# Kernel optimization log

Measured on AMD Instinct MI355X. Metric: run time of the kernel, lower is better.

The kernel has to match this reference:

```python
import jax, jax.numpy as jnp
import numpy as np

TOPK = 16  # matches selected per (frame, query pixel)


def setup_inputs() -> dict:
    key = jax.random.key(0)
    ks = jax.random.split(key, 4)
    B, T, N, C = 2, 3, 4096, 256  # batch, ref frames, 64x64 tokens, channels
    scale = 1.0 / np.sqrt(C)
    return {
        "tgt": jax.random.normal(ks[0], (B, N, C), dtype=jnp.float32),
        "ref": jax.random.normal(ks[1], (B, T, N, C), dtype=jnp.float32),
        "Wq": jax.random.normal(ks[2], (C, C), dtype=jnp.float32) * scale,
        "bq": jnp.zeros((C,), dtype=jnp.float32),
        "Wk": jax.random.normal(ks[3], (C, C), dtype=jnp.float32) * scale,
        "bk": jnp.zeros((C,), dtype=jnp.float32),
    }


def _l2norm(x, eps=1e-12):
    return x * jax.lax.rsqrt(jnp.sum(x * x, axis=-1, keepdims=True) + eps)


def reference(tgt, ref, Wq, bq, Wk, bk):
    # tgt: [B, Nq, C] target-frame tokens; ref: [B, T, Nr, C] reference-frame tokens
    B, Nq, C = tgt.shape
    T, Nr = ref.shape[1], ref.shape[2]
    q = _l2norm(tgt @ Wq + bq)                      # [B, Nq, C]
    k = _l2norm(ref @ Wk + bk)                      # [B, T, Nr, C]
    # cross-frame cosine-similarity correlation volume
    sim = jnp.einsum("bqc,btrc->btqr", q, k)        # [B, T, Nq, Nr]
    # top-k matched reference locations per query pixel
    topv, topi = jax.lax.top_k(sim, TOPK)           # [B, T, Nq, K]
    # gather matched reference features (irregular gather)
    bi = jnp.arange(B)[:, None, None, None]
    ti = jnp.arange(T)[None, :, None, None]
    gathered = ref[bi, ti, topi]                    # [B, T, Nq, K, C]
    # attention-weighted aggregation of matched features
    w = jax.nn.softmax(topv, axis=-1)               # [B, T, Nq, K]
    out = jnp.einsum("btqk,btqkc->btqc", w, gathered)  # [B, T, Nq, C]
    return out
```

## Files before the change

### kernel.cpp

```cpp
#include <hip/hip_runtime.h>
#include <stdint.h>

#define T_FRAMES 3
#define NTOK 4096
#define CH 256

typedef __attribute__((ext_vector_type(8))) short bf16x8;
typedef __attribute__((ext_vector_type(4))) float f32x4;
typedef __attribute__((address_space(1))) void gvoid;
typedef __attribute__((address_space(3))) void svoid;

__device__ __forceinline__ unsigned short f2bf_rne(float f) {
  union { float f; uint32_t u; } c; c.f = f;
  uint32_t u = c.u;
  return (unsigned short)((u + 0x7FFFu + ((u >> 16) & 1u)) >> 16);
}
__device__ __forceinline__ float bflo(uint32_t x) { return __uint_as_float(x << 16); }
__device__ __forceinline__ float bfhi(uint32_t x) { return __uint_as_float(x & 0xFFFF0000u); }

__global__ __launch_bounds__(256) void proj_kernel(
    const float* __restrict__ Xq, const float* __restrict__ Wq, const float* __restrict__ bq,
    const float* __restrict__ Xk, const float* __restrict__ Wk, const float* __restrict__ bk,
    unsigned short* __restrict__ Qb, float* __restrict__ Qlo,
    unsigned short* __restrict__ Kb, float* __restrict__ Klo)
{
  __shared__ double At[64][32];
  const int tid = threadIdx.x;
  int blk = blockIdx.x;
  const float *X, *W, *bias; unsigned short* Pb; float* Plo;
  if (blk < 256) { X = Xq; W = Wq; bias = bq; Pb = Qb; Plo = Qlo; }
  else           { X = Xk; W = Wk; bias = bk; Pb = Kb; Plo = Klo; blk -= 256; }
  const int rbase = blk * 32;
  const int wv = tid >> 6, lane = tid & 63;
  const int r0 = wv * 8;
  const int c4 = lane * 4;

  double acc[8][4];
  #pragma unroll
  for (int i = 0; i < 8; i++) {
    #pragma unroll
    for (int j = 0; j < 4; j++) acc[i][j] = (double)bias[c4 + j];
  }

  const int srow = tid & 31, skq = (tid >> 5) * 8;
  for (int kc = 0; kc < CH; kc += 64) {
    {
      const float* xp = X + (size_t)(rbase + srow) * CH + kc + skq;
      const float4 v0 = *(const float4*)(xp);
      const float4 v1 = *(const float4*)(xp + 4);
      At[skq + 0][srow] = (double)v0.x; At[skq + 1][srow] = (double)v0.y;
      At[skq + 2][srow] = (double)v0.z; At[skq + 3][srow] = (double)v0.w;
      At[skq + 4][srow] = (double)v1.x; At[skq + 5][srow] = (double)v1.y;
      At[skq + 6][srow] = (double)v1.z; At[skq + 7][srow] = (double)v1.w;
    }
    __syncthreads();
    #pragma unroll 8
    for (int k = 0; k < 64; k++) {
      const float4 w4 = *(const float4*)(W + (size_t)(kc + k) * CH + c4);
      const double b0 = (double)w4.x, b1 = (double)w4.y;
      const double b2 = (double)w4.z, b3 = (double)w4.w;
      double a[8];
      #pragma unroll
      for (int i = 0; i < 4; i++) {
        const double2 ap = *(const double2*)&At[k][r0 + 2 * i];
        a[2*i] = ap.x; a[2*i+1] = ap.y;
      }
      #pragma unroll
      for (int i = 0; i < 8; i++) {
        acc[i][0] += a[i] * b0; acc[i][1] += a[i] * b1;
        acc[i][2] += a[i] * b2; acc[i][3] += a[i] * b3;
      }
    }
    __syncthreads();
  }

  #pragma unroll
  for (int i = 0; i < 8; i++) {
    double ss = acc[i][0]*acc[i][0] + acc[i][1]*acc[i][1]
              + acc[i][2]*acc[i][2] + acc[i][3]*acc[i][3];
    #pragma unroll
    for (int off = 32; off >= 1; off >>= 1) ss += __shfl_xor(ss, off);
    const double inv = 1.0 / sqrt(ss + 1e-12);
    const size_t base = (size_t)(rbase + r0 + i) * CH + c4;
    double vd[4]; float fb[4]; unsigned short us[4];
    #pragma unroll
    for (int j = 0; j < 4; j++) {
      vd[j] = acc[i][j] * inv;
      us[j] = f2bf_rne((float)vd[j]);
      fb[j] = __uint_as_float(((uint32_t)us[j]) << 16);
    }
    uint2 pk; pk.x = (uint32_t)us[0] | ((uint32_t)us[1] << 16);
    pk.y = (uint32_t)us[2] | ((uint32_t)us[3] << 16);
    *(uint2*)(Pb + base) = pk;
    float4 lo;
    lo.x = (float)(vd[0] - (double)fb[0]); lo.y = (float)(vd[1] - (double)fb[1]);
    lo.z = (float)(vd[2] - (double)fb[2]); lo.w = (float)(vd[3] - (double)fb[3]);
    *(float4*)(Plo + base) = lo;
  }
}

__global__ __launch_bounds__(256, 4) void sim_cand_kernel(
    const unsigned short* __restrict__ Qb,
    const unsigned short* __restrict__ Kb,
    uint32_t* __restrict__ cand)
{
  __shared__ unsigned short kst[2][32 * 256];
  const int bid = blockIdx.x;
  const int rs = bid & 3;
  const int qb = (bid >> 2) & 63;
  const int bt = bid >> 8;
  const int b = bt / T_FRAMES;
  const int tid = threadIdx.x;
  const int wv = tid >> 6, lane = tid & 63;
  const int lq = lane & 15, g = lane >> 4;
  const int q = qb * 64 + wv * 16 + lq;

  bf16x8 bfr[8];
  {
    const unsigned short* qrow = Qb + (size_t)(b * NTOK + q) * CH + g * 8;
    #pragma unroll
    for (int kc = 0; kc < 8; kc++) bfr[kc] = *(const bf16x8*)(qrow + kc * 32);
  }
  uint32_t best[16];
  #pragma unroll
  for (int i = 0; i < 16; i++) best[i] = 0u;
  uint32_t s[16];

  const unsigned short* kbase = Kb + ((size_t)bt * NTOK + (size_t)rs * 1024) * CH;

#define STAGE(C, BUFI)                                                          \
  {                                                                             \
    _Pragma("unroll")                                                           \
    for (int t = 0; t < 4; t++) {                                               \
      const int o16 = (wv * 4 + t) * 64 + lane;                                 \
      const int row = o16 >> 5, colp = o16 & 31;                                \
      const int col16 = (colp - row) & 31;                                      \
      const unsigned short* gsrc = kbase + (size_t)((C) * 32 + row) * CH + col16 * 8; \
      __builtin_amdgcn_global_load_lds((const gvoid*)gsrc,                      \
          (svoid*)(&kst[BUFI][0] + (size_t)(wv * 4 + t) * 512), 16, 0, 0);      \
    }                                                                           \
  }

#define COMPUTE_HALF(CBASE, BUFI, SOFF)                                         \
  {                                                                             \
    _Pragma("unroll")                                                           \
    for (int t = 0; t < 2; t++) {                                               \
      f32x4 acc = {2.0f, 2.0f, 2.0f, 2.0f};                                     \
      const int arow = t * 16 + lq;                                             \
      const unsigned short* rowp = &kst[BUFI][0] + (size_t)arow * 256;          \
      _Pragma("unroll")                                                         \
      for (int kc = 0; kc < 8; kc++) {                                          \
        const int colp = (kc * 4 + g + arow) & 31;                              \
        const bf16x8 a = *(const bf16x8*)(rowp + colp * 8);                     \
        acc = __builtin_amdgcn_mfma_f32_16x16x32_bf16(a, bfr[kc], acc, 0, 0, 0);\
      }                                                                         \
      _Pragma("unroll")                                                         \
      for (int j = 0; j < 4; j++) {                                             \
        const uint32_t bits = __float_as_uint(acc[j]);                          \
        s[(SOFF) + t * 4 + j] = (bits & 0xFFFFFC00u) |                          \
            (uint32_t)((CBASE) * 32 + t * 16 + g * 4 + j);                      \
      }                                                                         \
    }                                                                           \
  }

#define SORT16_MERGE()                                                          \
  {                                                                             \
    _Pragma("unroll")                                                           \
    for (int bk = 2; bk <= 16; bk <<= 1) {                                      \
      _Pragma("unroll")                                                         \
      for (int bj = bk >> 1; bj > 0; bj >>= 1) {                                \
        _Pragma("unroll")                                                       \
        for (int i = 0; i < 16; i++) {                                          \
          const int l = i ^ bj;                                                 \
          if (l > i) {                                                          \
            const bool up = ((i & bk) != 0);                                    \
            const uint32_t a2 = s[i], b2 = s[l];                                \
            const uint32_t mn = a2 < b2 ? a2 : b2;                              \
            const uint32_t mx = a2 < b2 ? b2 : a2;                              \
            s[i] = up ? mn : mx; s[l] = up ? mx : mn;                           \
          }                                                                     \
        }                                                                       \
      }                                                                         \
    }                                                                           \
    uint32_t m[16];                                                             \
    _Pragma("unroll")                                                           \
    for (int i = 0; i < 16; i++) {                                              \
      const uint32_t a2 = best[i], b2 = s[15 - i];                              \
      m[i] = a2 > b2 ? a2 : b2;                                                 \
    }                                                                           \
    _Pragma("unroll")                                                           \
    for (int bj = 8; bj > 0; bj >>= 1) {                                        \
      _Pragma("unroll")                                                         \
      for (int i = 0; i < 16; i++) {                                            \
        const int l = i ^ bj;                                                   \
        if (l > i) {                                                            \
          const uint32_t a2 = m[i], b2 = m[l];                                  \
          const uint32_t mn = a2 < b2 ? a2 : b2;                                \
          const uint32_t mx = a2 < b2 ? b2 : a2;                                \
          m[i] = mx; m[l] = mn;                                                 \
        }                                                                       \
      }                                                                         \
    }                                                                           \
    _Pragma("unroll")                                                           \
    for (int i = 0; i < 16; i++) best[i] = m[i];                                \
  }

  STAGE(0, 0);
  __syncthreads();
  for (int cp = 0; cp < 16; cp++) {
    const int c0 = 2 * cp;
    STAGE(c0 + 1, 1);
    COMPUTE_HALF(c0, 0, 0);
    __syncthreads();
    if (cp < 15) STAGE(c0 + 2, 0);
    COMPUTE_HALF(c0 + 1, 1, 8);
    SORT16_MERGE();
    __syncthreads();
  }

  #pragma unroll
  for (int st = 16; st <= 32; st <<= 1) {
    uint32_t o[16];
    #pragma unroll
    for (int i = 0; i < 16; i++) o[i] = (uint32_t)__shfl_xor((int)best[15 - i], st);
    #pragma unroll
    for (int i = 0; i < 16; i++) best[i] = best[i] > o[i] ? best[i] : o[i];
    #pragma unroll
    for (int bj = 8; bj > 0; bj >>= 1) {
      #pragma unroll
      for (int i = 0; i < 16; i++) {
        const int l = i ^ bj;
        if (l > i) {
          const uint32_t a2 = best[i], b2 = best[l];
          const uint32_t mn = a2 < b2 ? a2 : b2;
          const uint32_t mx = a2 < b2 ? b2 : a2;
          best[i] = mx; best[l] = mn;
        }
      }
    }
  }
  if (g == 0) {
    uint32_t* cp2 = cand + ((size_t)bt * NTOK + q) * 64 + rs * 16;
    #pragma unroll
    for (int i = 0; i < 16; i += 4) {
      uint4 v; v.x = best[i]; v.y = best[i+1]; v.z = best[i+2]; v.w = best[i+3];
      *(uint4*)(cp2 + i) = v;
    }
  }
#undef STAGE
#undef COMPUTE_HALF
#undef SORT16_MERGE
}

__global__ __launch_bounds__(256) void out_kernel(
    const unsigned short* __restrict__ Qb, const float* __restrict__ Qlo,
    const unsigned short* __restrict__ Kb, const float* __restrict__ Klo,
    const uint32_t* __restrict__ cand, const float* __restrict__ ref,
    float* __restrict__ out)
{
  const int tid = threadIdx.x, wv = tid >> 6, lane = tid & 63;
  const int rowid = blockIdx.x * 4 + wv;
  const int bt = rowid >> 12, q = rowid & 4095;
  const int b = bt / T_FRAMES;

  const uint32_t k0 = cand[(size_t)rowid * 64 + lane];
  uint32_t key = (k0 & 0xFFFFF000u) | ((uint32_t)(lane >> 4) << 10) | (k0 & 0x3FFu);

  #pragma unroll
  for (int k = 2; k <= 64; k <<= 1) {
    #pragma unroll
    for (int j = k >> 1; j > 0; j >>= 1) {
      const uint32_t ok = (uint32_t)__shfl_xor((int)key, j);
      const bool takeMax = (((lane & j) != 0) == ((lane & k) == 0));
      if ((ok > key) == takeMax) key = ok;
    }
  }
  const float v = __uint_as_float(key & 0xFFFFF000u) - 2.0f;
  int rr = (int)(key & 0xFFFu);

  const float v16c = __shfl(v, 48);
  const float BW = 4.5e-3f;
  const bool band = fabsf(v - v16c) <= BW;

  const uint2 qbv = *(const uint2*)(Qb + (size_t)(b * NTOK + q) * CH + lane * 4);
  const float4 qlv = *(const float4*)(Qlo + (size_t)(b * NTOK + q) * CH + lane * 4);
  const double qd0 = (double)bflo(qbv.x) + (double)qlv.x;
  const double qd1 = (double)bfhi(qbv.x) + (double)qlv.y;
  const double qd2 = (double)bflo(qbv.y) + (double)qlv.z;
  const double qd3 = (double)bfhi(qbv.y) + (double)qlv.w;

  const unsigned short* kbp = Kb + (size_t)bt * NTOK * CH;
  const float* klp = Klo + (size_t)bt * NTOK * CH;

  double dval = -1.0e300;
  {
    const unsigned long long bm = __ballot(band);
    const int lo = __ffsll(bm) - 1;
    const int hi = 63 - __clzll(bm);
    for (int idx = lo; idx <= hi; idx++) {
      const int ri = __shfl(rr, idx);
      const uint2 kbv = *(const uint2*)(kbp + (size_t)ri * CH + lane * 4);
      const float4 klv = *(const float4*)(klp + (size_t)ri * CH + lane * 4);
      double dd = qd0 * ((double)bflo(kbv.x) + (double)klv.x)
                + qd1 * ((double)bfhi(kbv.x) + (double)klv.y)
                + qd2 * ((double)bflo(kbv.y) + (double)klv.z)
                + qd3 * ((double)bfhi(kbv.y) + (double)klv.w);
      #pragma unroll
      for (int off = 32; off >= 1; off >>= 1) dd += __shfl_xor(dd, off);
      if (lane == idx) dval = dd;
    }
  }
  double p = band ? dval : ((v > v16c + BW) ? (double)v : -1.0e300);

  #pragma unroll
  for (int k = 2; k <= 64; k <<= 1) {
    #pragma unroll
    for (int j = k >> 1; j > 0; j >>= 1) {
      const double op = __shfl_xor(p, j);
      const int orr = __shfl_xor(rr, j);
      const bool takeMax = (((lane & j) != 0) == ((lane & k) == 0));
      const bool og = (op > p) || (op == p && orr < rr);
      if (takeMax == og) { p = op; rr = orr; }
    }
  }

  double pm = p;
  #pragma unroll
  for (int j = 8; j >= 1; j >>= 1) pm = fmax(pm, __shfl_xor(pm, j));
  double e = (lane >= 48) ? exp(p - pm) : 0.0;
  double es = e;
  #pragma unroll
  for (int j = 8; j >= 1; j >>= 1) es += __shfl_xor(es, j);
  const float w = (float)(e / es);

  float a0 = 0.f, a1 = 0.f, a2 = 0.f, a3 = 0.f;
  const float* rbp = ref + (size_t)bt * NTOK * CH + lane * 4;
  #pragma unroll
  for (int i = 0; i < 16; i++) {
    const float wi = __shfl(w, 48 + i);
    const int ri = __shfl(rr, 48 + i) & 0xFFF;
    const float4 f = *(const float4*)(rbp + (size_t)ri * CH);
    a0 += wi * f.x; a1 += wi * f.y; a2 += wi * f.z; a3 += wi * f.w;
  }
  float4 o; o.x = a0; o.y = a1; o.z = a2; o.w = a3;
  *(float4*)(out + (size_t)rowid * CH + lane * 4) = o;
}

extern "C" void kernel_launch(void* const* d_in, const int* in_sizes, int n_in,
                              void* d_out, int out_size, void* d_ws, size_t ws_size,
                              hipStream_t stream) {
  const float* tgt = (const float*)d_in[0];
  const float* ref = (const float*)d_in[1];
  const float* Wq  = (const float*)d_in[2];
  const float* bq  = (const float*)d_in[3];
  const float* Wk  = (const float*)d_in[4];
  const float* bk  = (const float*)d_in[5];
  float* out = (float*)d_out;

  const int B = 2;
  const int RQ = B * NTOK;
  const int RK = B * T_FRAMES * NTOK;

  char* ws = (char*)d_ws;
  unsigned short* Qb = (unsigned short*)ws; ws += (size_t)RQ * CH * 2;
  float* Qlo = (float*)ws;                  ws += (size_t)RQ * CH * 4;
  unsigned short* Kb = (unsigned short*)ws; ws += (size_t)RK * CH * 2;
  float* Klo = (float*)ws;                  ws += (size_t)RK * CH * 4;
  uint32_t* cand = (uint32_t*)ws;           ws += (size_t)RK * 64 * 4;

  proj_kernel<<<RQ / 32 + RK / 32, 256, 0, stream>>>(
      tgt, Wq, bq, ref, Wk, bk, Qb, Qlo, Kb, Klo);
  sim_cand_kernel<<<6 * 64 * 4, 256, 0, stream>>>(Qb, Kb, cand);
  out_kernel<<<RK / 4, 256, 0, stream>>>(Qb, Qlo, Kb, Klo, cand, ref, out);
}
```

Before: 272.4 us.

## Gather fp16 copy of ref in out_kernel and remap blocks across XCDs

The projection kernel now also writes an fp16 copy of the reference features while it stages them. The output kernel gathers its top-k rows from that copy when the workspace is large enough, halving the bytes read per gathered row. Block indices in the output kernel are also remapped so that consecutive work items spread across the 8 XCDs, which is meant to improve L2 locality per frame. The cost is an extra write of ref in fp16 and reduced precision in the weighted aggregation, which may affect output accuracy.

Result: no change. 270.5 us (-0.7%).

```diff
diff --git a/kernel.cpp b/kernel.cpp
--- a/kernel.cpp
+++ b/kernel.cpp
@@ -1,4 +1,5 @@
 #include <hip/hip_runtime.h>
+#include <hip/hip_fp16.h>
 #include <stdint.h>
 
 #define T_FRAMES 3
@@ -22,18 +23,21 @@
     const float* __restrict__ Xq, const float* __restrict__ Wq, const float* __restrict__ bq,
     const float* __restrict__ Xk, const float* __restrict__ Wk, const float* __restrict__ bk,
     unsigned short* __restrict__ Qb, float* __restrict__ Qlo,
-    unsigned short* __restrict__ Kb, float* __restrict__ Klo)
+    unsigned short* __restrict__ Kb, float* __restrict__ Klo,
+    unsigned short* __restrict__ ref16)
 {
   __shared__ double At[64][32];
   const int tid = threadIdx.x;
   int blk = blockIdx.x;
   const float *X, *W, *bias; unsigned short* Pb; float* Plo;
-  if (blk < 256) { X = Xq; W = Wq; bias = bq; Pb = Qb; Plo = Qlo; }
-  else           { X = Xk; W = Wk; bias = bk; Pb = Kb; Plo = Klo; blk -= 256; }
+  bool isK;
+  if (blk < 256) { X = Xq; W = Wq; bias = bq; Pb = Qb; Plo = Qlo; isK = false; }
+  else           { X = Xk; W = Wk; bias = bk; Pb = Kb; Plo = Klo; isK = true; blk -= 256; }
   const int rbase = blk * 32;
   const int wv = tid >> 6, lane = tid & 63;
   const int r0 = wv * 8;
   const int c4 = lane * 4;
+  const bool e16 = isK && (ref16 != nullptr);
 
   double acc[8][4];
   #pragma unroll
@@ -52,6 +56,20 @@
       At[skq + 2][srow] = (double)v0.z; At[skq + 3][srow] = (double)v0.w;
       At[skq + 4][srow] = (double)v1.x; At[skq + 5][srow] = (double)v1.y;
       At[skq + 6][srow] = (double)v1.z; At[skq + 7][srow] = (double)v1.w;
+      if (e16) {
+        const uint32_t h0 = (uint32_t)__half_as_ushort(__float2half_rn(v0.x));
+        const uint32_t h1 = (uint32_t)__half_as_ushort(__float2half_rn(v0.y));
+        const uint32_t h2 = (uint32_t)__half_as_ushort(__float2half_rn(v0.z));
+        const uint32_t h3 = (uint32_t)__half_as_ushort(__float2half_rn(v0.w));
+        const uint32_t h4 = (uint32_t)__half_as_ushort(__float2half_rn(v1.x));
+        const uint32_t h5 = (uint32_t)__half_as_ushort(__float2half_rn(v1.y));
+        const uint32_t h6 = (uint32_t)__half_as_ushort(__float2half_rn(v1.z));
+        const uint32_t h7 = (uint32_t)__half_as_ushort(__float2half_rn(v1.w));
+        uint4 hv;
+        hv.x = h0 | (h1 << 16); hv.y = h2 | (h3 << 16);
+        hv.z = h4 | (h5 << 16); hv.w = h6 | (h7 << 16);
+        *(uint4*)(ref16 + (size_t)(rbase + srow) * CH + kc + skq) = hv;
+      }
     }
     __syncthreads();
     #pragma unroll 8
@@ -256,10 +274,13 @@
     const unsigned short* __restrict__ Qb, const float* __restrict__ Qlo,
     const unsigned short* __restrict__ Kb, const float* __restrict__ Klo,
     const uint32_t* __restrict__ cand, const float* __restrict__ ref,
+    const unsigned short* __restrict__ ref16, int use16,
     float* __restrict__ out)
 {
   const int tid = threadIdx.x, wv = tid >> 6, lane = tid & 63;
-  const int rowid = blockIdx.x * 4 + wv;
+  const int bid = blockIdx.x;
+  const int work = (bid & 7) * 768 + (bid >> 3);
+  const int rowid = work * 4 + wv;
   const int bt = rowid >> 12, q = rowid & 4095;
   const int b = bt / T_FRAMES;
 
@@ -334,13 +355,27 @@
   const float w = (float)(e / es);
 
   float a0 = 0.f, a1 = 0.f, a2 = 0.f, a3 = 0.f;
-  const float* rbp = ref + (size_t)bt * NTOK * CH + lane * 4;
-  #pragma unroll
-  for (int i = 0; i < 16; i++) {
-    const float wi = __shfl(w, 48 + i);
-    const int ri = __shfl(rr, 48 + i) & 0xFFF;
-    const float4 f = *(const float4*)(rbp + (size_t)ri * CH);
-    a0 += wi * f.x; a1 += wi * f.y; a2 += wi * f.z; a3 += wi * f.w;
+  if (use16) {
+    const unsigned short* rb16 = ref16 + (size_t)bt * NTOK * CH + lane * 4;
+    #pragma unroll
+    for (int i = 0; i < 16; i++) {
+      const float wi = __shfl(w, 48 + i);
+      const int ri = __shfl(rr, 48 + i) & 0xFFF;
+      const uint2 hv = *(const uint2*)(rb16 + (size_t)ri * CH);
+      a0 += wi * __half2float(__ushort_as_half((unsigned short)(hv.x & 0xFFFFu)));
+      a1 += wi * __half2float(__ushort_as_half((unsigned short)(hv.x >> 16)));
+      a2 += wi * __half2float(__ushort_as_half((unsigned short)(hv.y & 0xFFFFu)));
+      a3 += wi * __half2float(__ushort_as_half((unsigned short)(hv.y >> 16)));
+    }
+  } else {
+    const float* rbp = ref + (size_t)bt * NTOK * CH + lane * 4;
+    #pragma unroll
+    for (int i = 0; i < 16; i++) {
+      const float wi = __shfl(w, 48 + i);
+      const int ri = __shfl(rr, 48 + i) & 0xFFF;
+      const float4 f = *(const float4*)(rbp + (size_t)ri * CH);
+      a0 += wi * f.x; a1 += wi * f.y; a2 += wi * f.z; a3 += wi * f.w;
+    }
   }
   float4 o; o.x = a0; o.y = a1; o.z = a2; o.w = a3;
   *(float4*)(out + (size_t)rowid * CH + lane * 4) = o;
@@ -367,9 +402,12 @@
   unsigned short* Kb = (unsigned short*)ws; ws += (size_t)RK * CH * 2;
   float* Klo = (float*)ws;                  ws += (size_t)RK * CH * 4;
   uint32_t* cand = (uint32_t*)ws;           ws += (size_t)RK * 64 * 4;
+  const bool big = ws_size >= (size_t)69206016;
+  unsigned short* ref16 = big ? (unsigned short*)ws : nullptr;
+  const int use16 = big ? 1 : 0;
 
   proj_kernel<<<RQ / 32 + RK / 32, 256, 0, stream>>>(
-      tgt, Wq, bq, ref, Wk, bk, Qb, Qlo, Kb, Klo);
+      tgt, Wq, bq, ref, Wk, bk, Qb, Qlo, Kb, Klo, ref16);
   sim_cand_kernel<<<6 * 64 * 4, 256, 0, stream>>>(Qb, Kb, cand);
-  out_kernel<<<RK / 4, 256, 0, stream>>>(Qb, Qlo, Kb, Klo, cand, ref, out);
+  out_kernel<<<RK / 4, 256, 0, stream>>>(Qb, Qlo, Kb, Klo, cand, ref, ref16, use16, out);
 }
```
